# Performance work log

Hardware: AMD Instinct MI355X
Metric: run time of the kernel (lower is better)

Reference implementation:

```python
import jax, jax.numpy as jnp
import numpy as np

BN_EPS = 1e-5

def _gru_layer(x, w_ih, w_hh, b_ih, b_hh):
    # x: [B,T,I]; w_ih: [3H,I]; w_hh: [3H,H]; gate order r,z,n (PyTorch)
    B, T, _ = x.shape
    H = w_hh.shape[1]
    xw = jnp.einsum('bti,gi->btg', x, w_ih) + b_ih  # [B,T,3H], precompute input GEMM
    def step(h, xt):
        gh = h @ w_hh.T + b_hh
        xr, xz, xn = jnp.split(xt, 3, axis=-1)
        hr, hz, hn = jnp.split(gh, 3, axis=-1)
        r = jax.nn.sigmoid(xr + hr)
        z = jax.nn.sigmoid(xz + hz)
        n = jnp.tanh(xn + r * hn)
        h = (1.0 - z) * n + z * h
        return h, h
    h0 = jnp.zeros((B, H), x.dtype)
    _, hs = jax.lax.scan(step, h0, jnp.swapaxes(xw, 0, 1))  # [T,B,H]
    return jnp.swapaxes(hs, 0, 1)  # [B,T,H]

def _batchnorm_seq(x, gamma, beta):
    # BatchNorm1d over channels of [B,T,C]: stats over (B,T), biased var (training-mode math)
    mu = jnp.mean(x, axis=(0, 1))
    var = jnp.mean(jnp.square(x - mu), axis=(0, 1))
    return (x - mu) * jax.lax.rsqrt(var + BN_EPS) * gamma + beta

def setup_inputs() -> dict:
    key = jax.random.key(0)
    ks = jax.random.split(key, 16)
    B, T, I, H1, H2, O = 64, 1024, 64, 256, 256, 128
    s = lambda fan: 1.0 / np.sqrt(fan)
    u = lambda k, shp, fan: jax.random.uniform(k, shp, jnp.float32, -s(fan), s(fan))
    return {
        'x': jax.random.normal(ks[0], (B, T, I), jnp.float32),
        'w_ih1': u(ks[1], (3 * H1, I), H1), 'w_hh1': u(ks[2], (3 * H1, H1), H1),
        'b_ih1': u(ks[3], (3 * H1,), H1), 'b_hh1': u(ks[4], (3 * H1,), H1),
        'g1': 1.0 + 0.1 * jax.random.normal(ks[5], (H1,), jnp.float32),
        'be1': 0.1 * jax.random.normal(ks[6], (H1,), jnp.float32),
        'w_ih2': u(ks[7], (3 * H2, H1), H2), 'w_hh2': u(ks[8], (3 * H2, H2), H2),
        'b_ih2': u(ks[9], (3 * H2,), H2), 'b_hh2': u(ks[10], (3 * H2,), H2),
        'g2': 1.0 + 0.1 * jax.random.normal(ks[11], (H2,), jnp.float32),
        'be2': 0.1 * jax.random.normal(ks[12], (H2,), jnp.float32),
        'w_fc': u(ks[13], (O, H2), H2), 'b_fc': u(ks[14], (O,), H2),
    }

def reference(x, w_ih1, w_hh1, b_ih1, b_hh1, g1, be1,
              w_ih2, w_hh2, b_ih2, b_hh2, g2, be2, w_fc, b_fc):
    h = _gru_layer(x, w_ih1, w_hh1, b_ih1, b_hh1)
    h = _batchnorm_seq(h, g1, be1)  # dropout = identity (eval mode)
    h = _gru_layer(h, w_ih2, w_hh2, b_ih2, b_hh2)
    h = _batchnorm_seq(h, g2, be2)
    h = jnp.max(h, axis=1)          # global max pool over time -> [B,H2]
    h = jnp.tanh(h)
    return h @ w_fc.T + b_fc        # [B,O]
```

## Files before the change

kernel.cpp:

```cpp
#include <hip/hip_runtime.h>
#include <hip/hip_fp16.h>
#include <cstdint>
#include <cstddef>


#define DOT2(acc, w, h) \
    asm("v_dot2_f32_f16 %0, %1, %2, %0" : "+v"(acc) : "v"(w), "v"(h))

__device__ __forceinline__ void lds_barrier() {
    asm volatile("s_waitcnt lgkmcnt(0)\n\ts_barrier" ::: "memory");
}

__global__ void pack_whh(const float* __restrict__ w1, const float* __restrict__ w2,
                         __half2* __restrict__ o1, __half2* __restrict__ o2) {
    int g = blockIdx.x;
    int k2 = threadIdx.x;
    const float* w = blockIdx.y ? w2 : w1;
    __half2* o = blockIdx.y ? o2 : o1;
    float a = w[g * 256 + 2 * k2];
    float b = w[g * 256 + 2 * k2 + 1];
    o[g * 128 + k2] = __floats2half2_rn(a, b);
}

__global__ __launch_bounds__(256)
void gemm_xw1(const float* __restrict__ A, const float* __restrict__ W,
              const float* __restrict__ bias, __half* __restrict__ out) {
    __shared__ float As[64][65];
    __shared__ float Ws[64][65];
    const int tid = threadIdx.x;
    const int n0 = blockIdx.y * 64, g0 = blockIdx.x * 64;
    for (int idx = tid; idx < 4096; idx += 256) {
        int r = idx >> 6, c = idx & 63;
        As[r][c] = A[(size_t)(n0 + r) * 64 + c];
        Ws[r][c] = W[(size_t)(g0 + r) * 64 + c];
    }
    __syncthreads();
    const int ty = tid >> 4, tx = tid & 15;
    float acc[4][4] = {};
    for (int k = 0; k < 64; ++k) {
        float a[4], w[4];
        #pragma unroll
        for (int i = 0; i < 4; ++i) a[i] = As[ty * 4 + i][k];
        #pragma unroll
        for (int jj = 0; jj < 4; ++jj) w[jj] = Ws[tx * 4 + jj][k];
        #pragma unroll
        for (int i = 0; i < 4; ++i)
            #pragma unroll
            for (int jj = 0; jj < 4; ++jj) acc[i][jj] += a[i] * w[jj];
    }
    #pragma unroll
    for (int jj = 0; jj < 4; ++jj) {
        float bb = bias[g0 + tx * 4 + jj];
        #pragma unroll
        for (int i = 0; i < 4; ++i)
            out[(size_t)(n0 + ty * 4 + i) * 768 + (g0 + tx * 4 + jj)] =
                __float2half(acc[i][jj] + bb);
    }
}

__global__ __launch_bounds__(256)
void gemm_xw2(const __half2* __restrict__ A, const __half2* __restrict__ W,
              const float* __restrict__ bias, __half* __restrict__ out) {
    __shared__ __half2 As[64][33];
    __shared__ __half2 Ws[64][33];
    const int tid = threadIdx.x;
    const int n0 = blockIdx.y * 64, g0 = blockIdx.x * 64;
    const int ty = tid >> 4, tx = tid & 15;
    float acc[4][4] = {};
    for (int kc = 0; kc < 4; ++kc) {
        __syncthreads();
        for (int idx = tid; idx < 2048; idx += 256) {
            int r = idx >> 5, c2 = idx & 31;
            As[r][c2] = A[(size_t)(n0 + r) * 128 + kc * 32 + c2];
            Ws[r][c2] = W[(size_t)(g0 + r) * 128 + kc * 32 + c2];
        }
        __syncthreads();
        #pragma unroll 8
        for (int k2 = 0; k2 < 32; ++k2) {
            unsigned int a2[4], w2[4];
            #pragma unroll
            for (int i = 0; i < 4; ++i)
                a2[i] = __builtin_bit_cast(unsigned int, As[ty * 4 + i][k2]);
            #pragma unroll
            for (int jj = 0; jj < 4; ++jj)
                w2[jj] = __builtin_bit_cast(unsigned int, Ws[tx * 4 + jj][k2]);
            #pragma unroll
            for (int i = 0; i < 4; ++i)
                #pragma unroll
                for (int jj = 0; jj < 4; ++jj)
                    DOT2(acc[i][jj], w2[jj], a2[i]);
        }
    }
    #pragma unroll
    for (int jj = 0; jj < 4; ++jj) {
        float bb = bias[g0 + tx * 4 + jj];
        #pragma unroll
        for (int i = 0; i < 4; ++i)
            out[(size_t)(n0 + ty * 4 + i) * 768 + (g0 + tx * 4 + jj)] =
                __float2half(acc[i][jj] + bb);
    }
}

template<int LAYER>
__global__ __launch_bounds__(512, 2)
void rec_kernel(const __half2* __restrict__ wpack,
                const float* __restrict__ b_hh,
                const __half* __restrict__ xw,
                __half* __restrict__ y_out,
                float* __restrict__ stats,
                float* __restrict__ mx_out,
                float* __restrict__ mn_out) {
    __shared__ __align__(16) uint4 hbuf[2][2][17];
    const int tid = threadIdx.x;
    const int j  = tid >> 1;
    const int kq = tid & 1;
    const int b = blockIdx.x;

    uint4 wr[16], wz[16], wn[16];
    const uint4* wp4 = (const uint4*)wpack;
    const int wbase = kq * 16;
    #pragma unroll
    for (int m = 0; m < 16; ++m) wr[m] = wp4[(size_t)j * 32 + wbase + m];
    #pragma unroll
    for (int m = 0; m < 16; ++m) wz[m] = wp4[(size_t)(j + 256) * 32 + wbase + m];
    #pragma unroll
    for (int m = 0; m < 16; ++m) wn[m] = wp4[(size_t)(j + 512) * 32 + wbase + m];

    const float br = b_hh[j], bz = b_hh[256 + j], bn = b_hh[512 + j];

    if (tid < 34) ((uint4*)hbuf[0])[tid] = uint4{0u, 0u, 0u, 0u};

    float hprev = 0.f, ssum = 0.f, ssq = 0.f;
    float mx = -3.0e38f, mn = 3.0e38f;
    const __half* xwp = xw + (size_t)b * 1024 * 768;
    __half* yp = (LAYER == 1) ? (y_out + (size_t)b * 1024 * 256) : (__half*)nullptr;

    __half nxr = xwp[j], nxz = xwp[256 + j], nxn = xwp[512 + j];
    __syncthreads();

    for (int t = 0; t < 1024; ++t) {
        __half cxr = nxr, cxz = nxz, cxn = nxn;
        const __half* xq = xwp + (size_t)(t + 1) * 768;
        nxr = xq[j]; nxz = xq[256 + j]; nxn = xq[512 + j];

        float ar0 = 0.f, ar1 = 0.f, az0 = 0.f, az1 = 0.f, an0 = 0.f, an1 = 0.f;
        const uint4* hb = hbuf[t & 1][kq];
        #pragma unroll
        for (int m = 0; m < 16; ++m) {
            uint4 hq = hb[m];
            DOT2(ar0, wr[m].x, hq.x);
            DOT2(az0, wz[m].x, hq.x);
            DOT2(an0, wn[m].x, hq.x);
            DOT2(ar1, wr[m].y, hq.y);
            DOT2(az1, wz[m].y, hq.y);
            DOT2(an1, wn[m].y, hq.y);
            DOT2(ar0, wr[m].z, hq.z);
            DOT2(az0, wz[m].z, hq.z);
            DOT2(an0, wn[m].z, hq.z);
            DOT2(ar1, wr[m].w, hq.w);
            DOT2(az1, wz[m].w, hq.w);
            DOT2(an1, wn[m].w, hq.w);
        }
        float hr = ar0 + ar1, hz = az0 + az1, hn = an0 + an1;
        hr += __shfl_xor(hr, 1);
        hz += __shfl_xor(hz, 1);
        hn += __shfl_xor(hn, 1);
        hr += br; hz += bz; hn += bn;

        float xr = __half2float(cxr);
        float xz = __half2float(cxz);
        float xn = __half2float(cxn);
        float r = 1.f / (1.f + __expf(-(xr + hr)));
        float z = 1.f / (1.f + __expf(-(xz + hz)));
        float pa = xn + r * hn;
        pa = fminf(fmaxf(pa, -15.f), 15.f);
        float e2 = __expf(2.f * pa);
        float nn = (e2 - 1.f) / (e2 + 1.f);
        float h = (1.f - z) * nn + z * hprev;
        hprev = h;
        ssum += h;
        ssq += h * h;
        if (LAYER == 2) { mx = fmaxf(mx, h); mn = fminf(mn, h); }
        __half yh = __float2half(h);
        if (kq == 0) {
            ((__half*)hbuf[(t + 1) & 1][j >> 7])[j & 127] = yh;
            if (LAYER == 1) yp[(size_t)t * 256 + j] = yh;
        }
        lds_barrier();
    }
    if (kq == 0) {
        atomicAdd(&stats[j], ssum);
        atomicAdd(&stats[256 + j], ssq);
        if (LAYER == 2) {
            mx_out[b * 256 + j] = mx;
            mn_out[b * 256 + j] = mn;
        }
    }
}

__global__ void fold_bn1(const float* __restrict__ w_ih2, const float* __restrict__ b_ih2,
                         const float* __restrict__ g1, const float* __restrict__ be1,
                         const float* __restrict__ stats1,
                         __half* __restrict__ w_eff, float* __restrict__ b_eff) {
    const int g = blockIdx.x, lane = threadIdx.x;
    const float invN = 1.f / 65536.f;
    float partial = 0.f;
    for (int c = lane; c < 256; c += 64) {
        float mu = stats1[c] * invN;
        float var = stats1[256 + c] * invN - mu * mu;
        float s = g1[c] * rsqrtf(var + 1e-5f);
        float sh = be1[c] - mu * s;
        float w = w_ih2[g * 256 + c];
        w_eff[g * 256 + c] = __float2half(w * s);
        partial += w * sh;
    }
    #pragma unroll
    for (int off = 32; off > 0; off >>= 1) partial += __shfl_down(partial, off);
    if (lane == 0) b_eff[g] = b_ih2[g] + partial;
}

__global__ void final_kernel(const float* __restrict__ stats2,
                             const float* __restrict__ mx, const float* __restrict__ mn,
                             const float* __restrict__ g2, const float* __restrict__ be2,
                             const float* __restrict__ w_fc, const float* __restrict__ b_fc,
                             float* __restrict__ out) {
    __shared__ float v[256];
    const int b = blockIdx.x, c = threadIdx.x;
    const float invN = 1.f / 65536.f;
    float mu = stats2[c] * invN;
    float var = stats2[256 + c] * invN - mu * mu;
    float s = g2[c] * rsqrtf(var + 1e-5f);
    float d = be2[c] - mu * s;
    float M = (s >= 0.f) ? mx[b * 256 + c] : mn[b * 256 + c];
    v[c] = tanhf(s * M + d);
    __syncthreads();
    if (c < 128) {
        float acc = b_fc[c];
        for (int k = 0; k < 256; ++k) acc += v[k] * w_fc[c * 256 + k];
        out[b * 128 + c] = acc;
    }
}

extern "C" void kernel_launch(void* const* d_in, const int* in_sizes, int n_in,
                              void* d_out, int out_size, void* d_ws, size_t ws_size,
                              hipStream_t stream) {
    const float* x     = (const float*)d_in[0];
    const float* w_ih1 = (const float*)d_in[1];
    const float* w_hh1 = (const float*)d_in[2];
    const float* b_ih1 = (const float*)d_in[3];
    const float* b_hh1 = (const float*)d_in[4];
    const float* g1    = (const float*)d_in[5];
    const float* be1   = (const float*)d_in[6];
    const float* w_ih2 = (const float*)d_in[7];
    const float* w_hh2 = (const float*)d_in[8];
    const float* b_ih2 = (const float*)d_in[9];
    const float* b_hh2 = (const float*)d_in[10];
    const float* g2    = (const float*)d_in[11];
    const float* be2   = (const float*)d_in[12];
    const float* w_fc  = (const float*)d_in[13];
    const float* b_fc  = (const float*)d_in[14];
    float* out = (float*)d_out;

    char* ws = (char*)d_ws;
    size_t off = 0;
    __half*  xw   = (__half*)(ws + off);  off += (size_t)65536 * 768 * 2;
    __half*  y1   = (__half*)(ws + off);  off += (size_t)65536 * 256 * 2;
    __half2* wp1  = (__half2*)(ws + off); off += (size_t)768 * 128 * 4;
    __half2* wp2  = (__half2*)(ws + off); off += (size_t)768 * 128 * 4;
    __half*  weff = (__half*)(ws + off);  off += (size_t)768 * 256 * 2;
    float*   beff = (float*)(ws + off);   off += (size_t)768 * 4;
    float*   stats= (float*)(ws + off);   off += (size_t)1024 * 4;
    float*   mx2  = (float*)(ws + off);   off += (size_t)64 * 256 * 4;
    float*   mn2  = (float*)(ws + off);   off += (size_t)64 * 256 * 4;

    hipMemsetAsync(stats, 0, 4096, stream);

    pack_whh<<<dim3(768, 2), dim3(128), 0, stream>>>(w_hh1, w_hh2, wp1, wp2);
    gemm_xw1<<<dim3(12, 1024), dim3(256), 0, stream>>>(x, w_ih1, b_ih1, xw);
    rec_kernel<1><<<dim3(64), dim3(512), 0, stream>>>(wp1, b_hh1, xw, y1, stats,
                                                      (float*)nullptr, (float*)nullptr);
    fold_bn1<<<dim3(768), dim3(64), 0, stream>>>(w_ih2, b_ih2, g1, be1, stats, weff, beff);
    gemm_xw2<<<dim3(12, 1024), dim3(256), 0, stream>>>((const __half2*)y1, (const __half2*)weff,
                                                       beff, xw);
    rec_kernel<2><<<dim3(64), dim3(512), 0, stream>>>(wp2, b_hh2, xw, (__half*)nullptr,
                                                      stats + 512, mx2, mn2);
    final_kernel<<<dim3(64), dim3(256), 0, stream>>>(stats + 512, mx2, mn2, g2, be2,
                                                     w_fc, b_fc, out);
}
```

Baseline: 3.150 ms.

## Split GRU recurrent dot products four ways with two output units per thread

Each group of four threads now computes two hidden units over a quarter of the K dimension each, instead of two threads computing one unit over half of K. This halves LDS reads of h per dot product and shortens each thread's serial dot-product chain. The cost is a second shuffle reduction stage and more shuffles per step. The inline-asm dot2 is also replaced by the compiler builtin, which lets the compiler schedule it.

```diff
diff --git a/kernel.cpp b/kernel.cpp
--- a/kernel.cpp
+++ b/kernel.cpp
@@ -3,6 +3,13 @@
 #include <cstdint>
 #include <cstddef>
 
+
+typedef _Float16 half2_t __attribute__((ext_vector_type(2)));
+
+__device__ __forceinline__ float fdot2f(unsigned int w, unsigned int h, float acc) {
+    return __builtin_amdgcn_fdot2(__builtin_bit_cast(half2_t, w),
+                                  __builtin_bit_cast(half2_t, h), acc, false);
+}
 
 #define DOT2(acc, w, h) \
     asm("v_dot2_f32_f16 %0, %1, %2, %0" : "+v"(acc) : "v"(w), "v"(h))
@@ -110,62 +117,89 @@
                 float* __restrict__ stats,
                 float* __restrict__ mx_out,
                 float* __restrict__ mn_out) {
-    __shared__ __align__(16) uint4 hbuf[2][2][17];
+    __shared__ __align__(16) uint4 hb4[2][4][9];
     const int tid = threadIdx.x;
-    const int j  = tid >> 1;
-    const int kq = tid & 1;
-    const int b = blockIdx.x;
-
-    uint4 wr[16], wz[16], wn[16];
-    const uint4* wp4 = (const uint4*)wpack;
-    const int wbase = kq * 16;
-    #pragma unroll
-    for (int m = 0; m < 16; ++m) wr[m] = wp4[(size_t)j * 32 + wbase + m];
-    #pragma unroll
-    for (int m = 0; m < 16; ++m) wz[m] = wp4[(size_t)(j + 256) * 32 + wbase + m];
-    #pragma unroll
-    for (int m = 0; m < 16; ++m) wn[m] = wp4[(size_t)(j + 512) * 32 + wbase + m];
-
-    const float br = b_hh[j], bz = b_hh[256 + j], bn = b_hh[512 + j];
-
-    if (tid < 34) ((uint4*)hbuf[0])[tid] = uint4{0u, 0u, 0u, 0u};
+    const int p   = tid >> 2;
+    const int kq  = tid & 3;
+    const int kql = kq & 1;
+    const int u   = 2 * p + kql;
+    const int b   = blockIdx.x;
+
+    uint4 Wr0[8], Wr1[8], Wz0[8], Wz1[8], Wn0[8], Wn1[8];
+    {
+        const uint4* wp4 = (const uint4*)wpack;
+        const int mb = kq * 8;
+        #pragma unroll
+        for (int m = 0; m < 8; ++m) Wr0[m] = wp4[(size_t)(2 * p) * 32 + mb + m];
+        #pragma unroll
+        for (int m = 0; m < 8; ++m) Wr1[m] = wp4[(size_t)(2 * p + 1) * 32 + mb + m];
+        #pragma unroll
+        for (int m = 0; m < 8; ++m) Wz0[m] = wp4[(size_t)(2 * p + 256) * 32 + mb + m];
+        #pragma unroll
+        for (int m = 0; m < 8; ++m) Wz1[m] = wp4[(size_t)(2 * p + 257) * 32 + mb + m];
+        #pragma unroll
+        for (int m = 0; m < 8; ++m) Wn0[m] = wp4[(size_t)(2 * p + 512) * 32 + mb + m];
+        #pragma unroll
+        for (int m = 0; m < 8; ++m) Wn1[m] = wp4[(size_t)(2 * p + 513) * 32 + mb + m];
+    }
+
+    const float bru = b_hh[u], bzu = b_hh[256 + u], bnu = b_hh[512 + u];
+
+    if (tid < 36) ((uint4*)hb4)[tid] = uint4{0u, 0u, 0u, 0u};
 
     float hprev = 0.f, ssum = 0.f, ssq = 0.f;
     float mx = -3.0e38f, mn = 3.0e38f;
     const __half* xwp = xw + (size_t)b * 1024 * 768;
     __half* yp = (LAYER == 1) ? (y_out + (size_t)b * 1024 * 256) : (__half*)nullptr;
 
-    __half nxr = xwp[j], nxz = xwp[256 + j], nxn = xwp[512 + j];
+    __half nxr = xwp[u], nxz = xwp[256 + u], nxn = xwp[512 + u];
     __syncthreads();
 
     for (int t = 0; t < 1024; ++t) {
         __half cxr = nxr, cxz = nxz, cxn = nxn;
         const __half* xq = xwp + (size_t)(t + 1) * 768;
-        nxr = xq[j]; nxz = xq[256 + j]; nxn = xq[512 + j];
-
-        float ar0 = 0.f, ar1 = 0.f, az0 = 0.f, az1 = 0.f, an0 = 0.f, an1 = 0.f;
-        const uint4* hb = hbuf[t & 1][kq];
-        #pragma unroll
-        for (int m = 0; m < 16; ++m) {
-            uint4 hq = hb[m];
-            DOT2(ar0, wr[m].x, hq.x);
-            DOT2(az0, wz[m].x, hq.x);
-            DOT2(an0, wn[m].x, hq.x);
-            DOT2(ar1, wr[m].y, hq.y);
-            DOT2(az1, wz[m].y, hq.y);
-            DOT2(an1, wn[m].y, hq.y);
-            DOT2(ar0, wr[m].z, hq.z);
-            DOT2(az0, wz[m].z, hq.z);
-            DOT2(an0, wn[m].z, hq.z);
-            DOT2(ar1, wr[m].w, hq.w);
-            DOT2(az1, wz[m].w, hq.w);
-            DOT2(an1, wn[m].w, hq.w);
-        }
-        float hr = ar0 + ar1, hz = az0 + az1, hn = an0 + an1;
-        hr += __shfl_xor(hr, 1);
-        hz += __shfl_xor(hz, 1);
-        hn += __shfl_xor(hn, 1);
-        hr += br; hz += bz; hn += bn;
+        nxr = xq[u]; nxz = xq[256 + u]; nxn = xq[512 + u];
+
+        float r0 = 0.f, r1 = 0.f, z0 = 0.f, z1 = 0.f, n0 = 0.f, n1 = 0.f;
+        const uint4* hq = hb4[t & 1][kq];
+        #pragma unroll
+        for (int m = 0; m < 8; ++m) {
+            uint4 h = hq[m];
+            r0 = fdot2f(Wr0[m].x, h.x, r0);
+            r1 = fdot2f(Wr1[m].x, h.x, r1);
+            z0 = fdot2f(Wz0[m].x, h.x, z0);
+            z1 = fdot2f(Wz1[m].x, h.x, z1);
+            n0 = fdot2f(Wn0[m].x, h.x, n0);
+            n1 = fdot2f(Wn1[m].x, h.x, n1);
+            r0 = fdot2f(Wr0[m].y, h.y, r0);
+            r1 = fdot2f(Wr1[m].y, h.y, r1);
+            z0 = fdot2f(Wz0[m].y, h.y, z0);
+            z1 = fdot2f(Wz1[m].y, h.y, z1);
+            n0 = fdot2f(Wn0[m].y, h.y, n0);
+            n1 = fdot2f(Wn1[m].y, h.y, n1);
+            r0 = fdot2f(Wr0[m].z, h.z, r0);
+            r1 = fdot2f(Wr1[m].z, h.z, r1);
+            z0 = fdot2f(Wz0[m].z, h.z, z0);
+            z1 = fdot2f(Wz1[m].z, h.z, z1);
+            n0 = fdot2f(Wn0[m].z, h.z, n0);
+            n1 = fdot2f(Wn1[m].z, h.z, n1);
+            r0 = fdot2f(Wr0[m].w, h.w, r0);
+            r1 = fdot2f(Wr1[m].w, h.w, r1);
+            z0 = fdot2f(Wz0[m].w, h.w, z0);
+            z1 = fdot2f(Wz1[m].w, h.w, z1);
+            n0 = fdot2f(Wn0[m].w, h.w, n0);
+            n1 = fdot2f(Wn1[m].w, h.w, n1);
+        }
+        r0 += __shfl_xor(r0, 1); r0 += __shfl_xor(r0, 2);
+        r1 += __shfl_xor(r1, 1); r1 += __shfl_xor(r1, 2);
+        z0 += __shfl_xor(z0, 1); z0 += __shfl_xor(z0, 2);
+        z1 += __shfl_xor(z1, 1); z1 += __shfl_xor(z1, 2);
+        n0 += __shfl_xor(n0, 1); n0 += __shfl_xor(n0, 2);
+        n1 += __shfl_xor(n1, 1); n1 += __shfl_xor(n1, 2);
+
+        float hr = (kql ? r1 : r0) + bru;
+        float hz = (kql ? z1 : z0) + bzu;
+        float hn = (kql ? n1 : n0) + bnu;
 
         float xr = __half2float(cxr);
         float xz = __half2float(cxz);
@@ -182,18 +216,18 @@
         ssq += h * h;
         if (LAYER == 2) { mx = fmaxf(mx, h); mn = fminf(mn, h); }
         __half yh = __float2half(h);
-        if (kq == 0) {
-            ((__half*)hbuf[(t + 1) & 1][j >> 7])[j & 127] = yh;
-            if (LAYER == 1) yp[(size_t)t * 256 + j] = yh;
+        if (kq < 2) {
+            ((__half*)hb4[(t + 1) & 1][u >> 6])[u & 63] = yh;
+            if (LAYER == 1) yp[(size_t)t * 256 + u] = yh;
         }
         lds_barrier();
     }
-    if (kq == 0) {
-        atomicAdd(&stats[j], ssum);
-        atomicAdd(&stats[256 + j], ssq);
+    if (kq < 2) {
+        atomicAdd(&stats[u], ssum);
+        atomicAdd(&stats[256 + u], ssq);
         if (LAYER == 2) {
-            mx_out[b * 256 + j] = mx;
-            mn_out[b * 256 + j] = mn;
+            mx_out[b * 256 + u] = mx;
+            mn_out[b * 256 + u] = mn;
         }
     }
 }
```

New measurement: 3.043 ms. 1.04x faster.

## Compute GRU recurrent matvec with MFMA using register-resident weight fragments

Applied to the files above, without the earlier changes.

The recurrent h·W_hh product is rewritten from per-thread v_dot2 loops into 16x16x32 f16 MFMA instructions. Each wave keeps its slice of the r/z/n weights in registers as B fragments. The hidden state sits in a padded 16-row LDS tile where only row 0 is meaningful, so most of the MFMA work is spent on zero rows. This is meant to shorten the serial per-timestep latency by replacing many scalar dot2 ops with a few matrix ops. The gate math also switches to raw v_exp/v_rcp sigmoid and tanh, so only 16 lanes per wave do the elementwise update.

```diff
diff --git a/kernel.cpp b/kernel.cpp
--- a/kernel.cpp
+++ b/kernel.cpp
@@ -4,11 +4,32 @@
 #include <cstddef>
 
 
+typedef _Float16 f16x8 __attribute__((ext_vector_type(8)));
+typedef float f32x4 __attribute__((ext_vector_type(4)));
+
 #define DOT2(acc, w, h) \
     asm("v_dot2_f32_f16 %0, %1, %2, %0" : "+v"(acc) : "v"(w), "v"(h))
 
+#define PIN(x) asm volatile("" : "+v"(x))
+#define PIN4(q) do { PIN(q.x); PIN(q.y); PIN(q.z); PIN(q.w); } while (0)
+
 __device__ __forceinline__ void lds_barrier() {
     asm volatile("s_waitcnt lgkmcnt(0)\n\ts_barrier" ::: "memory");
+}
+
+__device__ __forceinline__ float fast_sigmoid(float x) {
+    float t = x * -1.4426950408889634f, e, r;
+    asm("v_exp_f32 %0, %1" : "=v"(e) : "v"(t));
+    float d = 1.f + e;
+    asm("v_rcp_f32 %0, %1" : "=v"(r) : "v"(d));
+    return r;
+}
+__device__ __forceinline__ float fast_tanh_clamped(float x) {
+    float t = x * 2.8853900817779268f, e, r;
+    asm("v_exp_f32 %0, %1" : "=v"(e) : "v"(t));
+    float d = e + 1.f;
+    asm("v_rcp_f32 %0, %1" : "=v"(r) : "v"(d));
+    return 1.f - 2.f * r;
 }
 
 __global__ void pack_whh(const float* __restrict__ w1, const float* __restrict__ w2,
@@ -110,90 +131,110 @@
                 float* __restrict__ stats,
                 float* __restrict__ mx_out,
                 float* __restrict__ mn_out) {
-    __shared__ __align__(16) uint4 hbuf[2][2][17];
+    __shared__ __align__(16) __half hb[2][16][264];
     const int tid = threadIdx.x;
-    const int j  = tid >> 1;
-    const int kq = tid & 1;
+    const int w = tid >> 6, l = tid & 63;
+    const int lm = l & 15, lk = l >> 4;
     const int b = blockIdx.x;
 
-    uint4 wr[16], wz[16], wn[16];
-    const uint4* wp4 = (const uint4*)wpack;
-    const int wbase = kq * 16;
-    #pragma unroll
-    for (int m = 0; m < 16; ++m) wr[m] = wp4[(size_t)j * 32 + wbase + m];
-    #pragma unroll
-    for (int m = 0; m < 16; ++m) wz[m] = wp4[(size_t)(j + 256) * 32 + wbase + m];
-    #pragma unroll
-    for (int m = 0; m < 16; ++m) wn[m] = wp4[(size_t)(j + 512) * 32 + wbase + m];
-
-    const float br = b_hh[j], bz = b_hh[256 + j], bn = b_hh[512 + j];
-
-    if (tid < 34) ((uint4*)hbuf[0])[tid] = uint4{0u, 0u, 0u, 0u};
-
-    float hprev = 0.f, ssum = 0.f, ssq = 0.f;
-    float mx = -3.0e38f, mn = 3.0e38f;
+    uint4 Bf[2][3][8];
+    {
+        const char* wbase = (const char*)wpack;
+        #pragma unroll
+        for (int sel = 0; sel < 2; ++sel)
+            #pragma unroll
+            for (int g = 0; g < 3; ++g)
+                #pragma unroll
+                for (int kt = 0; kt < 8; ++kt) {
+                    int gr = g * 256 + w * 32 + sel * 16 + lm;
+                    Bf[sel][g][kt] =
+                        *(const uint4*)(wbase + (size_t)gr * 512 + kt * 64 + lk * 16);
+                    PIN4(Bf[sel][g][kt]);
+                }
+    }
+
+    const int u0 = w * 32 + lm, u1 = u0 + 16;
+    const float br0 = b_hh[u0], bz0 = b_hh[256 + u0], bn0 = b_hh[512 + u0];
+    const float br1 = b_hh[u1], bz1 = b_hh[256 + u1], bn1 = b_hh[512 + u1];
+
+    for (int idx = tid; idx < 1056; idx += 512) ((uint4*)hb)[idx] = uint4{0u,0u,0u,0u};
+
+    float hp0 = 0.f, hp1 = 0.f;
+    float ssum0 = 0.f, ssq0 = 0.f, ssum1 = 0.f, ssq1 = 0.f;
+    float mx0 = -3e38f, mn0 = 3e38f, mx1 = -3e38f, mn1 = 3e38f;
     const __half* xwp = xw + (size_t)b * 1024 * 768;
-    __half* yp = (LAYER == 1) ? (y_out + (size_t)b * 1024 * 256) : (__half*)nullptr;
-
-    __half nxr = xwp[j], nxz = xwp[256 + j], nxn = xwp[512 + j];
+    __half* yp = y_out + (size_t)b * 1024 * 256;
+
+    __half nxr0 = xwp[u0], nxz0 = xwp[256 + u0], nxn0 = xwp[512 + u0];
+    __half nxr1 = xwp[u1], nxz1 = xwp[256 + u1], nxn1 = xwp[512 + u1];
     __syncthreads();
 
+    const char* hb_base = (const char*)hb;
+
     for (int t = 0; t < 1024; ++t) {
-        __half cxr = nxr, cxz = nxz, cxn = nxn;
+        __half cxr0 = nxr0, cxz0 = nxz0, cxn0 = nxn0;
+        __half cxr1 = nxr1, cxz1 = nxz1, cxn1 = nxn1;
         const __half* xq = xwp + (size_t)(t + 1) * 768;
-        nxr = xq[j]; nxz = xq[256 + j]; nxn = xq[512 + j];
-
-        float ar0 = 0.f, ar1 = 0.f, az0 = 0.f, az1 = 0.f, an0 = 0.f, an1 = 0.f;
-        const uint4* hb = hbuf[t & 1][kq];
-        #pragma unroll
-        for (int m = 0; m < 16; ++m) {
-            uint4 hq = hb[m];
-            DOT2(ar0, wr[m].x, hq.x);
-            DOT2(az0, wz[m].x, hq.x);
-            DOT2(an0, wn[m].x, hq.x);
-            DOT2(ar1, wr[m].y, hq.y);
-            DOT2(az1, wz[m].y, hq.y);
-            DOT2(an1, wn[m].y, hq.y);
-            DOT2(ar0, wr[m].z, hq.z);
-            DOT2(az0, wz[m].z, hq.z);
-            DOT2(an0, wn[m].z, hq.z);
-            DOT2(ar1, wr[m].w, hq.w);
-            DOT2(az1, wz[m].w, hq.w);
-            DOT2(an1, wn[m].w, hq.w);
-        }
-        float hr = ar0 + ar1, hz = az0 + az1, hn = an0 + an1;
-        hr += __shfl_xor(hr, 1);
-        hz += __shfl_xor(hz, 1);
-        hn += __shfl_xor(hn, 1);
-        hr += br; hz += bz; hn += bn;
-
-        float xr = __half2float(cxr);
-        float xz = __half2float(cxz);
-        float xn = __half2float(cxn);
-        float r = 1.f / (1.f + __expf(-(xr + hr)));
-        float z = 1.f / (1.f + __expf(-(xz + hz)));
-        float pa = xn + r * hn;
-        pa = fminf(fmaxf(pa, -15.f), 15.f);
-        float e2 = __expf(2.f * pa);
-        float nn = (e2 - 1.f) / (e2 + 1.f);
-        float h = (1.f - z) * nn + z * hprev;
-        hprev = h;
-        ssum += h;
-        ssq += h * h;
-        if (LAYER == 2) { mx = fmaxf(mx, h); mn = fminf(mn, h); }
-        __half yh = __float2half(h);
-        if (kq == 0) {
-            ((__half*)hbuf[(t + 1) & 1][j >> 7])[j & 127] = yh;
-            if (LAYER == 1) yp[(size_t)t * 256 + j] = yh;
+        nxr0 = xq[u0]; nxz0 = xq[256 + u0]; nxn0 = xq[512 + u0];
+        nxr1 = xq[u1]; nxz1 = xq[256 + u1]; nxn1 = xq[512 + u1];
+
+        const size_t abase = (size_t)(t & 1) * 8448 + (size_t)lm * 528 + lk * 16;
+        __half* hwr = &hb[(t + 1) & 1][0][0];
+
+        #pragma unroll
+        for (int sel = 0; sel < 2; ++sel) {
+            f32x4 ar = {0.f, 0.f, 0.f, 0.f};
+            f32x4 az = {0.f, 0.f, 0.f, 0.f};
+            f32x4 an = {0.f, 0.f, 0.f, 0.f};
+            #pragma unroll
+            for (int kt = 0; kt < 8; ++kt) {
+                f16x8 a = *(const f16x8*)(hb_base + abase + kt * 64);
+                ar = __builtin_amdgcn_mfma_f32_16x16x32_f16(
+                        a, __builtin_bit_cast(f16x8, Bf[sel][0][kt]), ar, 0, 0, 0);
+                az = __builtin_amdgcn_mfma_f32_16x16x32_f16(
+                        a, __builtin_bit_cast(f16x8, Bf[sel][1][kt]), az, 0, 0, 0);
+                an = __builtin_amdgcn_mfma_f32_16x16x32_f16(
+                        a, __builtin_bit_cast(f16x8, Bf[sel][2][kt]), an, 0, 0, 0);
+            }
+            if (l < 16) {
+                float xr = __half2float(sel ? cxr1 : cxr0);
+                float xz = __half2float(sel ? cxz1 : cxz0);
+                float xn = __half2float(sel ? cxn1 : cxn0);
+                float hr = ar[0] + (sel ? br1 : br0);
+                float hz = az[0] + (sel ? bz1 : bz0);
+                float hn = an[0] + (sel ? bn1 : bn0);
+                float r = fast_sigmoid(xr + hr);
+                float z = fast_sigmoid(xz + hz);
+                float pa = xn + r * hn;
+                pa = fminf(fmaxf(pa, -15.f), 15.f);
+                float nn = fast_tanh_clamped(pa);
+                float hprev = sel ? hp1 : hp0;
+                float h = (1.f - z) * nn + z * hprev;
+                int u = sel ? u1 : u0;
+                if (sel) {
+                    hp1 = h; ssum1 += h; ssq1 += h * h;
+                    if (LAYER == 2) { mx1 = fmaxf(mx1, h); mn1 = fminf(mn1, h); }
+                } else {
+                    hp0 = h; ssum0 += h; ssq0 += h * h;
+                    if (LAYER == 2) { mx0 = fmaxf(mx0, h); mn0 = fminf(mn0, h); }
+                }
+                __half yh = __float2half(h);
+                hwr[u] = yh;
+                if (LAYER == 1) yp[(size_t)t * 256 + u] = yh;
+            }
         }
         lds_barrier();
     }
-    if (kq == 0) {
-        atomicAdd(&stats[j], ssum);
-        atomicAdd(&stats[256 + j], ssq);
+    if (l < 16) {
+        atomicAdd(&stats[u0], ssum0);
+        atomicAdd(&stats[256 + u0], ssq0);
+        atomicAdd(&stats[u1], ssum1);
+        atomicAdd(&stats[256 + u1], ssq1);
         if (LAYER == 2) {
-            mx_out[b * 256 + j] = mx;
-            mn_out[b * 256 + j] = mn;
+            mx_out[b * 256 + u0] = mx0;
+            mn_out[b * 256 + u0] = mn0;
+            mx_out[b * 256 + u1] = mx1;
+            mn_out[b * 256 + u1] = mn1;
         }
     }
 }
@@ -273,7 +314,7 @@
     float*   mx2  = (float*)(ws + off);   off += (size_t)64 * 256 * 4;
     float*   mn2  = (float*)(ws + off);   off += (size_t)64 * 256 * 4;
 
-    hipMemsetAsync(stats, 0, 4096, stream);
+    (void)hipMemsetAsync(stats, 0, 4096, stream);
 
     pack_whh<<<dim3(768, 2), dim3(128), 0, stream>>>(w_hh1, w_hh2, wp1, wp2);
     gemm_xw1<<<dim3(12, 1024), dim3(256), 0, stream>>>(x, w_ih1, b_ih1, xw);
@@ -282,7 +323,7 @@
     fold_bn1<<<dim3(768), dim3(64), 0, stream>>>(w_ih2, b_ih2, g1, be1, stats, weff, beff);
     gemm_xw2<<<dim3(12, 1024), dim3(256), 0, stream>>>((const __half2*)y1, (const __half2*)weff,
                                                        beff, xw);
-    rec_kernel<2><<<dim3(64), dim3(512), 0, stream>>>(wp2, b_hh2, xw, (__half*)nullptr,
+    rec_kernel<2><<<dim3(64), dim3(512), 0, stream>>>(wp2, b_hh2, xw, y1,
                                                       stats + 512, mx2, mn2);
     final_kernel<<<dim3(64), dim3(256), 0, stream>>>(stats + 512, mx2, mn2, g2, be2,
                                                      w_fc, b_fc, out);
```

Result: slower. 4.153 ms (+31.8%).
